# Performance work log

Hardware: AMD Instinct MI355X
Metric: run time of the kernel (lower is better)

Reference implementation:

```python
import jax, jax.numpy as jnp
import numpy as np

# Dimensions
T, B, N, E = 16, 16, 1024, 16384   # seq len, graphs per step, nodes/graph, edges/graph
F_IN, MID, H = 128, 16, 256        # node features, GCN mid channels, hidden_dim
RATIO = 0.8
K = int(np.ceil(RATIO * N))        # SAGPooling keeps K=820 nodes per graph


def setup_inputs() -> dict:
    key = jax.random.key(0)
    ks = jax.random.split(key, 16)
    def p(k, shape, s=0.05):
        return jax.random.normal(k, shape, dtype=jnp.float32) * s
    return {
        "x": jax.random.normal(ks[0], (T, B, N, F_IN), dtype=jnp.float32),
        "edge_index": jax.random.randint(ks[1], (T, B, 2, E), 0, N, dtype=jnp.int32),
        "conv1_W": p(ks[2], (F_IN, MID)),
        "conv1_b": p(ks[3], (MID,)),
        "sag_Wl": p(ks[4], (MID, 1)),   # GraphConv lin_rel (neighbor aggregate)
        "sag_Wr": p(ks[5], (MID, 1)),   # GraphConv lin_root (self)
        "sag_b": p(ks[6], (1,)),
        "conv2_W": p(ks[7], (MID, H)),
        "conv2_b": p(ks[8], (H,)),
        "W_ih": p(ks[9], (4 * H, H)),   # LSTM gates in PyTorch order i,f,g,o
        "W_hh": p(ks[10], (4 * H, H)),
        "b_ih": p(ks[11], (4 * H,)),
        "b_hh": p(ks[12], (4 * H,)),
        "cls_W": p(ks[13], (H, 1)),
        "cls_b": p(ks[14], (1,)),
    }


def _gcn(x, src, dst, w, W, b, n):
    # GCNConv with self-loops: out_i = sum_j d_i^-1/2 d_j^-1/2 w_ij (x_j W) + d_i^-1 (x_i W) + b
    h = x @ W                                            # [n, out]
    deg = jnp.ones((n,), x.dtype).at[dst].add(w)         # +1 for self-loop weight
    dinv = jax.lax.rsqrt(deg)
    coef = dinv[src] * dinv[dst] * w                     # [e]
    out = jnp.zeros_like(h).at[dst].add(h[src] * coef[:, None])
    return out + h * (dinv * dinv)[:, None] + b


def _graph_embed(x, ei, conv1_W, conv1_b, sag_Wl, sag_Wr, sag_b, conv2_W, conv2_b):
    src, dst = ei[0], ei[1]
    w = jnp.ones((E,), x.dtype)
    # conv1 + relu
    h1 = jax.nn.relu(_gcn(x, src, dst, w, conv1_W, conv1_b, N))
    # SAGPooling score via GraphConv(16 -> 1): sum-aggregate neighbors + root
    agg = jnp.zeros_like(h1).at[dst].add(h1[src])
    score = (agg @ sag_Wl + h1 @ sag_Wr + sag_b)[:, 0]   # [N]
    sv, perm = jax.lax.top_k(score, K)                   # top-k nodes
    xp = h1[perm] * jnp.tanh(sv)[:, None]                # gate kept nodes
    # remap edges to kept-node ids; drop edges touching removed nodes via zero weight
    newidx = jnp.full((N,), -1, jnp.int32).at[perm].set(jnp.arange(K, dtype=jnp.int32))
    ns, nd = newidx[src], newidx[dst]
    valid = (ns >= 0) & (nd >= 0)
    ew = valid.astype(x.dtype)
    ns = jnp.where(valid, ns, 0)
    nd = jnp.where(valid, nd, 0)
    # conv2 + relu, then global mean pool over the K kept nodes
    h2 = jax.nn.relu(_gcn(xp, ns, nd, ew, conv2_W, conv2_b, K))
    return h2.mean(axis=0)                               # [H]


def reference(x, edge_index, conv1_W, conv1_b, sag_Wl, sag_Wr, sag_b,
              conv2_W, conv2_b, W_ih, W_hh, b_ih, b_hh, cls_W, cls_b):
    embed = lambda xg, eg: _graph_embed(xg, eg, conv1_W, conv1_b,
                                        sag_Wl, sag_Wr, sag_b, conv2_W, conv2_b)
    emb = jax.vmap(jax.vmap(embed))(x, edge_index)       # [T, B, H]

    def step(carry, xt):
        h, c = carry
        g = xt @ W_ih.T + b_ih + h @ W_hh.T + b_hh
        i, f, gg, o = jnp.split(g, 4, axis=-1)
        c = jax.nn.sigmoid(f) * c + jax.nn.sigmoid(i) * jnp.tanh(gg)
        h = jax.nn.sigmoid(o) * jnp.tanh(c)
        return (h, c), None

    h0 = jnp.zeros((B, H), x.dtype)
    (hT, _), _ = jax.lax.scan(step, (h0, h0), emb)       # hT = lstm_out[:, -1, :]
    return hT @ cls_W + cls_b                            # [B, 1]
```

## Files before the change

### kernel.cpp

```cpp
#include <hip/hip_runtime.h>
#include <cmath>

#define TT 16
#define BB 16
#define NN 1024
#define EE 16384
#define FIN 128
#define MIDC 16
#define HH 256
#define KK 820
#define HS 20

#define OFF_HBUF   0
#define N_HBUF     (NN*HS)
#define OFF_CSR    (OFF_HBUF + N_HBUF)
#define N_CSR      (EE/2)
#define OFF_HEAD   (OFF_CSR + N_CSR)
#define OFF_CUR    (OFF_HEAD + NN + 1)
#define OFF_SCANA  (OFF_CUR + NN)
#define OFF_DINV   (OFF_SCANA + NN)
#define OFF_UB     (OFF_DINV + NN)
#define OFF_HIST   (OFF_UB + NN)
#define OFF_S      (OFF_HIST + 256)
#define OFF_WCNT   (OFF_S + 256)
#define OFF_CTRL   (OFF_WCNT + 16)
#define SM_FLOATS  (OFF_CTRL + 8)
#define SM_BYTES   (SM_FLOATS * 4)

__global__ __launch_bounds__(1024) void k_graph(
    const float* __restrict__ x, const int* __restrict__ ei,
    const float* __restrict__ W1, const float* __restrict__ b1,
    const float* __restrict__ Wl, const float* __restrict__ Wr,
    const float* __restrict__ bsag, const float* __restrict__ W2,
    const float* __restrict__ b2, float* __restrict__ emb)
{
  extern __shared__ __align__(16) float sm[];
  float*          hbuf  = sm + OFF_HBUF;
  float4*         hb4   = (float4*)hbuf;
  unsigned short* csr   = (unsigned short*)(sm + OFF_CSR);
  int*            head  = (int*)(sm + OFF_HEAD);
  int*            cur   = (int*)(sm + OFF_CUR);
  int*            scanA = (int*)(sm + OFF_SCANA);
  int*            scanB = (int*)(sm + OFF_DINV);
  float*          dinvb = sm + OFF_DINV;
  unsigned*       ubv   = (unsigned*)(sm + OFF_UB);
  int*            hist  = (int*)(sm + OFF_HIST);
  int*            S     = (int*)(sm + OFF_S);
  int*            wcnt  = (int*)(sm + OFF_WCNT);
  int*            ctrl  = (int*)(sm + OFF_CTRL);

  const int g   = blockIdx.x;
  const int tid = threadIdx.x;
  const float* xg   = x  + (size_t)g * (NN*FIN);
  const int*   srcp = ei + (size_t)g * (2*EE);
  const int*   dstp = srcp + EE;

  cur[tid] = 0;

  float hown[MIDC];
  {
    const float4* xr = (const float4*)(xg + (size_t)tid * FIN);
#pragma unroll
    for (int c = 0; c < MIDC; ++c) hown[c] = 0.0f;
    for (int k4 = 0; k4 < FIN/4; ++k4) {
      float4 v = xr[k4];
      const float* w0 = W1 + (k4*4 + 0)*MIDC;
      const float* w1 = W1 + (k4*4 + 1)*MIDC;
      const float* w2 = W1 + (k4*4 + 2)*MIDC;
      const float* w3 = W1 + (k4*4 + 3)*MIDC;
#pragma unroll
      for (int c = 0; c < MIDC; ++c)
        hown[c] += v.x*w0[c] + v.y*w1[c] + v.z*w2[c] + v.w*w3[c];
    }
    hb4[tid*5+0] = make_float4(hown[0],  hown[1],  hown[2],  hown[3]);
    hb4[tid*5+1] = make_float4(hown[4],  hown[5],  hown[6],  hown[7]);
    hb4[tid*5+2] = make_float4(hown[8],  hown[9],  hown[10], hown[11]);
    hb4[tid*5+3] = make_float4(hown[12], hown[13], hown[14], hown[15]);
  }
  __syncthreads();

  for (int e = tid; e < EE; e += 1024) atomicAdd(&cur[dstp[e]], 1);
  __syncthreads();

  {
    int v = cur[tid];
    scanA[tid] = v;
    __syncthreads();
    int* s_ = scanA; int* d_ = scanB;
    for (int off = 1; off < NN; off <<= 1) {
      int t = s_[tid];
      if (tid >= off) t += s_[tid - off];
      d_[tid] = t;
      __syncthreads();
      int* tmp = s_; s_ = d_; d_ = tmp;
    }
    int inc = s_[tid];
    int ex  = inc - v;
    __syncthreads();
    head[tid] = ex;
    cur[tid]  = ex;
    if (tid == 0) head[NN] = EE;
    dinvb[tid] = rsqrtf((float)(v + 1));
  }
  __syncthreads();

  for (int e = tid; e < EE; e += 1024) {
    int s = srcp[e], d = dstp[e];
    int pos = atomicAdd(&cur[d], 1);
    csr[pos] = (unsigned short)s;
  }
  __syncthreads();

  const int beg = head[tid], end = head[tid+1];

  float h1own[MIDC];
  {
    float accv[MIDC];
#pragma unroll
    for (int c = 0; c < MIDC; ++c) accv[c] = 0.0f;
    for (int p = beg; p < end; ++p) {
      int s = csr[p];
      float ds_ = dinvb[s];
      float4 a0 = hb4[s*5+0], a1 = hb4[s*5+1], a2 = hb4[s*5+2], a3 = hb4[s*5+3];
      accv[0]  += a0.x*ds_; accv[1]  += a0.y*ds_; accv[2]  += a0.z*ds_; accv[3]  += a0.w*ds_;
      accv[4]  += a1.x*ds_; accv[5]  += a1.y*ds_; accv[6]  += a1.z*ds_; accv[7]  += a1.w*ds_;
      accv[8]  += a2.x*ds_; accv[9]  += a2.y*ds_; accv[10] += a2.z*ds_; accv[11] += a2.w*ds_;
      accv[12] += a3.x*ds_; accv[13] += a3.y*ds_; accv[14] += a3.z*ds_; accv[15] += a3.w*ds_;
    }
    float di = dinvb[tid];
#pragma unroll
    for (int c = 0; c < MIDC; ++c)
      h1own[c] = fmaxf(di*accv[c] + hown[c]*di*di + b1[c], 0.0f);
  }
  __syncthreads();
  hb4[tid*5+0] = make_float4(h1own[0],  h1own[1],  h1own[2],  h1own[3]);
  hb4[tid*5+1] = make_float4(h1own[4],  h1own[5],  h1own[6],  h1own[7]);
  hb4[tid*5+2] = make_float4(h1own[8],  h1own[9],  h1own[10], h1own[11]);
  hb4[tid*5+3] = make_float4(h1own[12], h1own[13], h1own[14], h1own[15]);
  __syncthreads();

  float score;
  unsigned myu;
  {
    float aggv[MIDC];
#pragma unroll
    for (int c = 0; c < MIDC; ++c) aggv[c] = 0.0f;
    for (int p = beg; p < end; ++p) {
      int s = csr[p];
      float4 a0 = hb4[s*5+0], a1 = hb4[s*5+1], a2 = hb4[s*5+2], a3 = hb4[s*5+3];
      aggv[0]  += a0.x; aggv[1]  += a0.y; aggv[2]  += a0.z; aggv[3]  += a0.w;
      aggv[4]  += a1.x; aggv[5]  += a1.y; aggv[6]  += a1.z; aggv[7]  += a1.w;
      aggv[8]  += a2.x; aggv[9]  += a2.y; aggv[10] += a2.z; aggv[11] += a2.w;
      aggv[12] += a3.x; aggv[13] += a3.y; aggv[14] += a3.z; aggv[15] += a3.w;
    }
    score = bsag[0];
#pragma unroll
    for (int c = 0; c < MIDC; ++c) score += aggv[c]*Wl[c] + h1own[c]*Wr[c];
    unsigned ubits = __float_as_uint(score);
    myu = (ubits & 0x80000000u) ? ~ubits : (ubits | 0x80000000u);
  }

  int remK = KK;
  unsigned pref = 0;
  for (int byte = 3; byte >= 0; --byte) {
    if (tid < 256) hist[tid] = 0;
    __syncthreads();
    const int sh = byte * 8;
    const unsigned hi_mask = (byte == 3) ? 0u : (0xFFFFFFFFu << (sh + 8));
    if ((myu & hi_mask) == pref) atomicAdd(&hist[(myu >> sh) & 255u], 1);
    __syncthreads();
    if (tid < 64) {
      int h0 = hist[tid*4+0], h1_ = hist[tid*4+1], h2_ = hist[tid*4+2], h3_ = hist[tid*4+3];
      int s3 = h3_, s2 = h2_ + s3, s1 = h1_ + s2, s0 = h0 + s1;
      int run = s0;
#pragma unroll
      for (int off = 1; off < 64; off <<= 1) {
        int o = __shfl_down(run, off);
        if (tid + off < 64) run += o;
      }
      int above = run - s0;
      S[tid*4+0] = above + s0;
      S[tid*4+1] = above + s1;
      S[tid*4+2] = above + s2;
      S[tid*4+3] = above + s3;
    }
    __syncthreads();
    if (tid < 256) {
      int Sv = S[tid];
      int Sn = (tid < 255) ? S[tid+1] : 0;
      if (Sv >= remK && Sn < remK) { ctrl[0] = remK - Sn; ctrl[1] = tid; }
    }
    __syncthreads();
    remK  = ctrl[0];
    pref |= ((unsigned)ctrl[1]) << sh;
    __syncthreads();
  }
  const unsigned vstar = pref;
  const int need = remK;

  {
    const int wid = tid >> 6, lane = tid & 63;
    bool eq = (myu == vstar);
    unsigned long long m = __ballot(eq);
    if (lane == 0) wcnt[wid] = __popcll(m);
    __syncthreads();
    int before = (lane == 0) ? 0 : __popcll(m & ((~0ull) >> (64 - lane)));
    for (int w = 0; w < wid; ++w) before += wcnt[w];
    int kept = (myu > vstar) ? 1 : (eq ? (before < need) : 0);
    float gate = kept ? tanhf(score) : 0.0f;
#pragma unroll
    for (int c = 0; c < MIDC; ++c) h1own[c] *= gate;
    hb4[tid*5+0] = make_float4(h1own[0],  h1own[1],  h1own[2],  h1own[3]);
    hb4[tid*5+1] = make_float4(h1own[4],  h1own[5],  h1own[6],  h1own[7]);
    hb4[tid*5+2] = make_float4(h1own[8],  h1own[9],  h1own[10], h1own[11]);
    hb4[tid*5+3] = make_float4(h1own[12], h1own[13], h1own[14], h1own[15]);
    ubv[tid] = (unsigned)kept;
  }
  __syncthreads();

  float di2;
  {
    int cnt2 = 0;
    for (int p = beg; p < end; ++p) cnt2 += (int)ubv[csr[p]];
    di2 = rsqrtf((float)(1 + cnt2));
    dinvb[tid] = di2;
  }
  __syncthreads();

  {
    float acc2[MIDC];
#pragma unroll
    for (int c = 0; c < MIDC; ++c) acc2[c] = 0.0f;
    for (int p = beg; p < end; ++p) {
      int s = csr[p];
      float ds_ = dinvb[s];
      float4 a0 = hb4[s*5+0], a1 = hb4[s*5+1], a2 = hb4[s*5+2], a3 = hb4[s*5+3];
      acc2[0]  += a0.x*ds_; acc2[1]  += a0.y*ds_; acc2[2]  += a0.z*ds_; acc2[3]  += a0.w*ds_;
      acc2[4]  += a1.x*ds_; acc2[5]  += a1.y*ds_; acc2[6]  += a1.z*ds_; acc2[7]  += a1.w*ds_;
      acc2[8]  += a2.x*ds_; acc2[9]  += a2.y*ds_; acc2[10] += a2.z*ds_; acc2[11] += a2.w*ds_;
      acc2[12] += a3.x*ds_; acc2[13] += a3.y*ds_; acc2[14] += a3.z*ds_; acc2[15] += a3.w*ds_;
    }
#pragma unroll
    for (int c = 0; c < MIDC; ++c)
      h1own[c] = di2*acc2[c] + h1own[c]*di2*di2;
  }
  __syncthreads();
  hb4[tid*5+0] = make_float4(h1own[0],  h1own[1],  h1own[2],  h1own[3]);
  hb4[tid*5+1] = make_float4(h1own[4],  h1own[5],  h1own[6],  h1own[7]);
  hb4[tid*5+2] = make_float4(h1own[8],  h1own[9],  h1own[10], h1own[11]);
  hb4[tid*5+3] = make_float4(h1own[12], h1own[13], h1own[14], h1own[15]);
  __syncthreads();

  {
    const int ig = tid >> 6, h4 = tid & 63;
    float4 w2c[MIDC];
#pragma unroll
    for (int c = 0; c < MIDC; ++c) w2c[c] = *(const float4*)(W2 + c*HH + (h4 << 2));
    float4 bv = *(const float4*)(b2 + (h4 << 2));
    float4 pacc = make_float4(0.f, 0.f, 0.f, 0.f);
    for (int k = 0; k < 64; ++k) {
      int i = (ig << 6) + k;
      if (ubv[i] == 0u) continue;
      float4 v0 = hb4[i*5+0], v1 = hb4[i*5+1], v2 = hb4[i*5+2], v3 = hb4[i*5+3];
      float vv[MIDC] = {v0.x,v0.y,v0.z,v0.w, v1.x,v1.y,v1.z,v1.w,
                        v2.x,v2.y,v2.z,v2.w, v3.x,v3.y,v3.z,v3.w};
      float t0 = bv.x, t1 = bv.y, t2 = bv.z, t3 = bv.w;
#pragma unroll
      for (int c = 0; c < MIDC; ++c) {
        t0 += vv[c]*w2c[c].x; t1 += vv[c]*w2c[c].y;
        t2 += vv[c]*w2c[c].z; t3 += vv[c]*w2c[c].w;
      }
      pacc.x += fmaxf(t0, 0.f); pacc.y += fmaxf(t1, 0.f);
      pacc.z += fmaxf(t2, 0.f); pacc.w += fmaxf(t3, 0.f);
    }
    float4* part4 = (float4*)(sm + OFF_CSR);
    part4[(ig << 6) + h4] = pacc;
  }
  __syncthreads();
  if (tid < HH) {
    const float* part = sm + OFF_CSR;
    float s = 0.f;
#pragma unroll
    for (int ig = 0; ig < 16; ++ig) s += part[ig*HH + tid];
    emb[(size_t)g*HH + tid] = s * (1.0f/(float)KK);
  }
}

__global__ __launch_bounds__(1024) void k_gatepre(
    const float* __restrict__ emb, const float* __restrict__ W_ih,
    const float* __restrict__ b_ih, const float* __restrict__ b_hh,
    float* __restrict__ A)
{
  __shared__ __align__(16) float es[HH];
  const int g = blockIdx.x, tid = threadIdx.x;
  const int wid = tid >> 6, lane = tid & 63;
  const int sub = lane & 15, rq = lane >> 4;
  if (tid < HH) es[tid] = emb[(size_t)g*HH + tid];
  __syncthreads();
  const float4* e4 = (const float4*)es;
  for (int it = 0; it < 16; ++it) {
    const int j = it*64 + wid*4 + rq;
    const float4* wr = (const float4*)(W_ih + (size_t)j*HH);
    float p = 0.f;
#pragma unroll
    for (int kk = 0; kk < 4; ++kk) {
      float4 w = wr[sub + 16*kk];
      float4 e = e4[sub + 16*kk];
      p += w.x*e.x + w.y*e.y + w.z*e.z + w.w*e.w;
    }
    p += __shfl_xor(p, 1); p += __shfl_xor(p, 2);
    p += __shfl_xor(p, 4); p += __shfl_xor(p, 8);
    if (sub == 0) A[(size_t)g*1024 + j] = p + b_ih[j] + b_hh[j];
  }
}

__global__ __launch_bounds__(256) void k_step(
    const float* __restrict__ A_t, const float* __restrict__ W_hh,
    const float* __restrict__ h_in, float* __restrict__ h_out,
    float* __restrict__ cbuf)
{
  __shared__ __align__(16) float hsh[HH];
  __shared__ float gl[16][4];
  const int b = blockIdx.x >> 4, ug = blockIdx.x & 15;
  const int tid = threadIdx.x;
  const int ul = tid >> 4, sub = tid & 15;
  if (tid < HH) hsh[tid] = h_in[b*HH + tid];
  __syncthreads();
  const float4* h4 = (const float4*)hsh;
  float4 hv0 = h4[sub], hv1 = h4[sub+16], hv2 = h4[sub+32], hv3 = h4[sub+48];
  const int u = ug*16 + ul;
  float gv[4];
#pragma unroll
  for (int gg_ = 0; gg_ < 4; ++gg_) {
    const float4* wr = (const float4*)(W_hh + (size_t)(gg_*HH + u)*HH);
    float4 w0 = wr[sub], w1 = wr[sub+16], w2 = wr[sub+32], w3 = wr[sub+48];
    float p = w0.x*hv0.x + w0.y*hv0.y + w0.z*hv0.z + w0.w*hv0.w
            + w1.x*hv1.x + w1.y*hv1.y + w1.z*hv1.z + w1.w*hv1.w
            + w2.x*hv2.x + w2.y*hv2.y + w2.z*hv2.z + w2.w*hv2.w
            + w3.x*hv3.x + w3.y*hv3.y + w3.z*hv3.z + w3.w*hv3.w;
    p += __shfl_xor(p, 1); p += __shfl_xor(p, 2);
    p += __shfl_xor(p, 4); p += __shfl_xor(p, 8);
    gv[gg_] = p;
  }
  if (sub == 0) { gl[ul][0]=gv[0]; gl[ul][1]=gv[1]; gl[ul][2]=gv[2]; gl[ul][3]=gv[3]; }
  __syncthreads();
  if (tid < 16) {
    const int uu = ug*16 + tid;
    const float* At = A_t + b*1024;
    float gi = gl[tid][0] + At[uu      ];
    float gf = gl[tid][1] + At[uu + 256];
    float gn = gl[tid][2] + At[uu + 512];
    float go = gl[tid][3] + At[uu + 768];
    float iv = 1.0f/(1.0f + expf(-gi));
    float fv = 1.0f/(1.0f + expf(-gf));
    float gvv = tanhf(gn);
    float ov = 1.0f/(1.0f + expf(-go));
    float c = fv * cbuf[b*HH + uu] + iv * gvv;
    cbuf[b*HH + uu] = c;
    h_out[b*HH + uu] = ov * tanhf(c);
  }
}

__global__ __launch_bounds__(256) void k_cls(
    const float* __restrict__ h, const float* __restrict__ cls_W,
    const float* __restrict__ cls_b, float* __restrict__ out)
{
  __shared__ float red[4];
  const int b = blockIdx.x, tid = threadIdx.x;
  float p = h[b*HH + tid] * cls_W[tid];
#pragma unroll
  for (int off = 32; off >= 1; off >>= 1) p += __shfl_down(p, off);
  if ((tid & 63) == 0) red[tid >> 6] = p;
  __syncthreads();
  if (tid == 0) out[b] = red[0] + red[1] + red[2] + red[3] + cls_b[0];
}

extern "C" void kernel_launch(void* const* d_in, const int* in_sizes, int n_in,
                              void* d_out, int out_size, void* d_ws, size_t ws_size,
                              hipStream_t stream)
{
  const float* x    = (const float*)d_in[0];
  const int*   ei   = (const int*)  d_in[1];
  const float* W1   = (const float*)d_in[2];
  const float* b1   = (const float*)d_in[3];
  const float* Wl   = (const float*)d_in[4];
  const float* Wr   = (const float*)d_in[5];
  const float* bs   = (const float*)d_in[6];
  const float* W2   = (const float*)d_in[7];
  const float* b2   = (const float*)d_in[8];
  const float* Wih  = (const float*)d_in[9];
  const float* Whh  = (const float*)d_in[10];
  const float* bih  = (const float*)d_in[11];
  const float* bhh  = (const float*)d_in[12];
  const float* clsW = (const float*)d_in[13];
  const float* clsb = (const float*)d_in[14];
  float* out = (float*)d_out;

  float* emb = (float*)d_ws;
  float* A   = emb + (size_t)TT*BB*HH;
  float* hA  = emb;
  float* hB  = emb + BB*HH;
  float* cb  = emb + 2*BB*HH;

  (void)hipFuncSetAttribute(reinterpret_cast<const void*>(k_graph),
      hipFuncAttributeMaxDynamicSharedMemorySize, SM_BYTES);

  hipLaunchKernelGGL(k_graph, dim3(TT*BB), dim3(1024), SM_BYTES, stream,
                     x, ei, W1, b1, Wl, Wr, bs, W2, b2, emb);
  hipLaunchKernelGGL(k_gatepre, dim3(TT*BB), dim3(1024), 0, stream,
                     emb, Wih, bih, bhh, A);
  (void)hipMemsetAsync(hA, 0, BB*HH*sizeof(float), stream);
  (void)hipMemsetAsync(cb, 0, BB*HH*sizeof(float), stream);
  for (int t = 0; t < TT; ++t) {
    const float* hin  = (t & 1) ? hB : hA;
    float*       hout = (t & 1) ? hA : hB;
    hipLaunchKernelGGL(k_step, dim3(256), dim3(256), 0, stream,
                       A + (size_t)t*BB*1024, Whh, hin, hout, cb);
  }
  hipLaunchKernelGGL(k_cls, dim3(BB), dim3(256), 0, stream, hA, clsW, clsb, out);
}
```

Baseline: 423.2 us.

## Split conv1 into bf16 kernel and fuse LSTM into persistent grid-barrier kernel

The x@W1 projection moves out of the graph kernel into a separate fully parallel kernel that writes bf16-packed results. The graph kernel then reads 32 bytes per node instead of recomputing the projection from 512 bytes. The gate precompute, the 16 LSTM step launches and the classifier are merged into one persistent kernel that keeps W_ih/W_hh rows in registers and syncs with a software grid barrier, removing about 18 launches. Risks: bf16 rounding of h1 may change which nodes top-k selects, and the grid barrier assumes all 256 blocks are co-resident.

```diff
diff --git a/kernel.cpp b/kernel.cpp
--- a/kernel.cpp
+++ b/kernel.cpp
@@ -27,16 +27,56 @@
 #define SM_FLOATS  (OFF_CTRL + 8)
 #define SM_BYTES   (SM_FLOATS * 4)
 
+__device__ __forceinline__ unsigned bf16pair(float a, float b) {
+  unsigned ua = __float_as_uint(a), ub_ = __float_as_uint(b);
+  ua  = (ua  + 0x7FFFu + ((ua  >> 16) & 1u)) >> 16;
+  ub_ = (ub_ + 0x7FFFu + ((ub_ >> 16) & 1u)) >> 16;
+  return ua | (ub_ << 16);
+}
+__device__ __forceinline__ float bf16lo(unsigned p) { return __uint_as_float(p << 16); }
+__device__ __forceinline__ float bf16hi(unsigned p) { return __uint_as_float(p & 0xFFFF0000u); }
+__device__ __forceinline__ float dot4(float4 a, float4 b) {
+  return a.x*b.x + a.y*b.y + a.z*b.z + a.w*b.w;
+}
+
+__global__ __launch_bounds__(256) void k_conv1(
+    const float* __restrict__ x, const float* __restrict__ W1,
+    unsigned* __restrict__ h0)
+{
+  const int gid = blockIdx.x * 256 + threadIdx.x;
+  const float4* xr = (const float4*)(x + (size_t)gid * FIN);
+  float acc[MIDC];
+#pragma unroll
+  for (int c = 0; c < MIDC; ++c) acc[c] = 0.0f;
+  for (int k4 = 0; k4 < FIN/4; ++k4) {
+    float4 v = xr[k4];
+    const float* w0 = W1 + (k4*4 + 0)*MIDC;
+    const float* w1 = W1 + (k4*4 + 1)*MIDC;
+    const float* w2 = W1 + (k4*4 + 2)*MIDC;
+    const float* w3 = W1 + (k4*4 + 3)*MIDC;
+#pragma unroll
+    for (int c = 0; c < MIDC; ++c)
+      acc[c] += v.x*w0[c] + v.y*w1[c] + v.z*w2[c] + v.w*w3[c];
+  }
+  uint4 q0, q1;
+  q0.x = bf16pair(acc[0],  acc[1]);  q0.y = bf16pair(acc[2],  acc[3]);
+  q0.z = bf16pair(acc[4],  acc[5]);  q0.w = bf16pair(acc[6],  acc[7]);
+  q1.x = bf16pair(acc[8],  acc[9]);  q1.y = bf16pair(acc[10], acc[11]);
+  q1.z = bf16pair(acc[12], acc[13]); q1.w = bf16pair(acc[14], acc[15]);
+  uint4* o = (uint4*)h0;
+  o[(size_t)gid*2 + 0] = q0;
+  o[(size_t)gid*2 + 1] = q1;
+}
+
 __global__ __launch_bounds__(1024) void k_graph(
-    const float* __restrict__ x, const int* __restrict__ ei,
-    const float* __restrict__ W1, const float* __restrict__ b1,
+    const unsigned* __restrict__ h0, const int* __restrict__ ei,
+    const float* __restrict__ b1,
     const float* __restrict__ Wl, const float* __restrict__ Wr,
     const float* __restrict__ bsag, const float* __restrict__ W2,
     const float* __restrict__ b2, float* __restrict__ emb)
 {
   extern __shared__ __align__(16) float sm[];
-  float*          hbuf  = sm + OFF_HBUF;
-  float4*         hb4   = (float4*)hbuf;
+  float4*         hb4   = (float4*)(sm + OFF_HBUF);
   unsigned short* csr   = (unsigned short*)(sm + OFF_CSR);
   int*            head  = (int*)(sm + OFF_HEAD);
   int*            cur   = (int*)(sm + OFF_CUR);
@@ -51,7 +91,6 @@
 
   const int g   = blockIdx.x;
   const int tid = threadIdx.x;
-  const float* xg   = x  + (size_t)g * (NN*FIN);
   const int*   srcp = ei + (size_t)g * (2*EE);
   const int*   dstp = srcp + EE;
 
@@ -59,19 +98,16 @@
 
   float hown[MIDC];
   {
-    const float4* xr = (const float4*)(xg + (size_t)tid * FIN);
-#pragma unroll
-    for (int c = 0; c < MIDC; ++c) hown[c] = 0.0f;
-    for (int k4 = 0; k4 < FIN/4; ++k4) {
-      float4 v = xr[k4];
-      const float* w0 = W1 + (k4*4 + 0)*MIDC;
-      const float* w1 = W1 + (k4*4 + 1)*MIDC;
-      const float* w2 = W1 + (k4*4 + 2)*MIDC;
-      const float* w3 = W1 + (k4*4 + 3)*MIDC;
-#pragma unroll
-      for (int c = 0; c < MIDC; ++c)
-        hown[c] += v.x*w0[c] + v.y*w1[c] + v.z*w2[c] + v.w*w3[c];
-    }
+    const uint4* hp = (const uint4*)h0 + (size_t)g * NN * 2;
+    uint4 p0 = hp[tid*2], p1 = hp[tid*2 + 1];
+    hown[0] = bf16lo(p0.x); hown[1] = bf16hi(p0.x);
+    hown[2] = bf16lo(p0.y); hown[3] = bf16hi(p0.y);
+    hown[4] = bf16lo(p0.z); hown[5] = bf16hi(p0.z);
+    hown[6] = bf16lo(p0.w); hown[7] = bf16hi(p0.w);
+    hown[8]  = bf16lo(p1.x); hown[9]  = bf16hi(p1.x);
+    hown[10] = bf16lo(p1.y); hown[11] = bf16hi(p1.y);
+    hown[12] = bf16lo(p1.z); hown[13] = bf16hi(p1.z);
+    hown[14] = bf16lo(p1.w); hown[15] = bf16hi(p1.w);
     hb4[tid*5+0] = make_float4(hown[0],  hown[1],  hown[2],  hown[3]);
     hb4[tid*5+1] = make_float4(hown[4],  hown[5],  hown[6],  hown[7]);
     hb4[tid*5+2] = make_float4(hown[8],  hown[9],  hown[10], hown[11]);
@@ -170,8 +206,8 @@
     if ((myu & hi_mask) == pref) atomicAdd(&hist[(myu >> sh) & 255u], 1);
     __syncthreads();
     if (tid < 64) {
-      int h0 = hist[tid*4+0], h1_ = hist[tid*4+1], h2_ = hist[tid*4+2], h3_ = hist[tid*4+3];
-      int s3 = h3_, s2 = h2_ + s3, s1 = h1_ + s2, s0 = h0 + s1;
+      int h0_ = hist[tid*4+0], h1_ = hist[tid*4+1], h2_ = hist[tid*4+2], h3_ = hist[tid*4+3];
+      int s3 = h3_, s2 = h2_ + s3, s1 = h1_ + s2, s0 = h0_ + s1;
       int run = s0;
 #pragma unroll
       for (int off = 1; off < 64; off <<= 1) {
@@ -286,93 +322,110 @@
   }
 }
 
-__global__ __launch_bounds__(1024) void k_gatepre(
+__device__ __forceinline__ void grid_barrier(unsigned* bar, unsigned nblk) {
+  __syncthreads();
+  if (threadIdx.x == 0) {
+    __threadfence();
+    unsigned g0 = __hip_atomic_load(bar + 1, __ATOMIC_RELAXED, __HIP_MEMORY_SCOPE_AGENT);
+    unsigned arr = __hip_atomic_fetch_add(bar, 1u, __ATOMIC_ACQ_REL, __HIP_MEMORY_SCOPE_AGENT);
+    if (arr == nblk - 1u) {
+      __hip_atomic_store(bar, 0u, __ATOMIC_RELAXED, __HIP_MEMORY_SCOPE_AGENT);
+      __hip_atomic_fetch_add(bar + 1, 1u, __ATOMIC_RELEASE, __HIP_MEMORY_SCOPE_AGENT);
+    } else {
+      while (__hip_atomic_load(bar + 1, __ATOMIC_ACQUIRE, __HIP_MEMORY_SCOPE_AGENT) == g0)
+        __builtin_amdgcn_s_sleep(8);
+    }
+    __threadfence();
+  }
+  __syncthreads();
+}
+
+__global__ __launch_bounds__(256) void k_lstm_all(
     const float* __restrict__ emb, const float* __restrict__ W_ih,
     const float* __restrict__ b_ih, const float* __restrict__ b_hh,
-    float* __restrict__ A)
+    const float* __restrict__ W_hh, const float* __restrict__ clsW,
+    const float* __restrict__ clsb, float* __restrict__ hA,
+    float* __restrict__ hB, unsigned* __restrict__ bar,
+    float* __restrict__ out)
 {
-  __shared__ __align__(16) float es[HH];
-  const int g = blockIdx.x, tid = threadIdx.x;
-  const int wid = tid >> 6, lane = tid & 63;
-  const int sub = lane & 15, rq = lane >> 4;
-  if (tid < HH) es[tid] = emb[(size_t)g*HH + tid];
-  __syncthreads();
-  const float4* e4 = (const float4*)es;
-  for (int it = 0; it < 16; ++it) {
-    const int j = it*64 + wid*4 + rq;
-    const float4* wr = (const float4*)(W_ih + (size_t)j*HH);
-    float p = 0.f;
-#pragma unroll
-    for (int kk = 0; kk < 4; ++kk) {
-      float4 w = wr[sub + 16*kk];
-      float4 e = e4[sub + 16*kk];
-      p += w.x*e.x + w.y*e.y + w.z*e.z + w.w*e.w;
-    }
-    p += __shfl_xor(p, 1); p += __shfl_xor(p, 2);
-    p += __shfl_xor(p, 4); p += __shfl_xor(p, 8);
-    if (sub == 0) A[(size_t)g*1024 + j] = p + b_ih[j] + b_hh[j];
-  }
-}
-
-__global__ __launch_bounds__(256) void k_step(
-    const float* __restrict__ A_t, const float* __restrict__ W_hh,
-    const float* __restrict__ h_in, float* __restrict__ h_out,
-    float* __restrict__ cbuf)
-{
-  __shared__ __align__(16) float hsh[HH];
-  __shared__ float gl[16][4];
-  const int b = blockIdx.x >> 4, ug = blockIdx.x & 15;
-  const int tid = threadIdx.x;
-  const int ul = tid >> 4, sub = tid & 15;
-  if (tid < HH) hsh[tid] = h_in[b*HH + tid];
-  __syncthreads();
-  const float4* h4 = (const float4*)hsh;
-  float4 hv0 = h4[sub], hv1 = h4[sub+16], hv2 = h4[sub+32], hv3 = h4[sub+48];
+  __shared__ float Ablk[TT][4][16];
+  __shared__ float redsc[4];
+  const int bid = blockIdx.x, b = bid >> 4, ug = bid & 15;
+  const int tid = threadIdx.x, ul = tid >> 4, sub = tid & 15;
   const int u = ug*16 + ul;
-  float gv[4];
-#pragma unroll
-  for (int gg_ = 0; gg_ < 4; ++gg_) {
-    const float4* wr = (const float4*)(W_hh + (size_t)(gg_*HH + u)*HH);
-    float4 w0 = wr[sub], w1 = wr[sub+16], w2 = wr[sub+32], w3 = wr[sub+48];
-    float p = w0.x*hv0.x + w0.y*hv0.y + w0.z*hv0.z + w0.w*hv0.w
-            + w1.x*hv1.x + w1.y*hv1.y + w1.z*hv1.z + w1.w*hv1.w
-            + w2.x*hv2.x + w2.y*hv2.y + w2.z*hv2.z + w2.w*hv2.w
-            + w3.x*hv3.x + w3.y*hv3.y + w3.z*hv3.z + w3.w*hv3.w;
-    p += __shfl_xor(p, 1); p += __shfl_xor(p, 2);
-    p += __shfl_xor(p, 4); p += __shfl_xor(p, 8);
-    gv[gg_] = p;
-  }
-  if (sub == 0) { gl[ul][0]=gv[0]; gl[ul][1]=gv[1]; gl[ul][2]=gv[2]; gl[ul][3]=gv[3]; }
-  __syncthreads();
-  if (tid < 16) {
-    const int uu = ug*16 + tid;
-    const float* At = A_t + b*1024;
-    float gi = gl[tid][0] + At[uu      ];
-    float gf = gl[tid][1] + At[uu + 256];
-    float gn = gl[tid][2] + At[uu + 512];
-    float go = gl[tid][3] + At[uu + 768];
-    float iv = 1.0f/(1.0f + expf(-gi));
-    float fv = 1.0f/(1.0f + expf(-gf));
-    float gvv = tanhf(gn);
-    float ov = 1.0f/(1.0f + expf(-go));
-    float c = fv * cbuf[b*HH + uu] + iv * gvv;
-    cbuf[b*HH + uu] = c;
-    h_out[b*HH + uu] = ov * tanhf(c);
-  }
-}
-
-__global__ __launch_bounds__(256) void k_cls(
-    const float* __restrict__ h, const float* __restrict__ cls_W,
-    const float* __restrict__ cls_b, float* __restrict__ out)
-{
-  __shared__ float red[4];
-  const int b = blockIdx.x, tid = threadIdx.x;
-  float p = h[b*HH + tid] * cls_W[tid];
-#pragma unroll
-  for (int off = 32; off >= 1; off >>= 1) p += __shfl_down(p, off);
-  if ((tid & 63) == 0) red[tid >> 6] = p;
-  __syncthreads();
-  if (tid == 0) out[b] = red[0] + red[1] + red[2] + red[3] + cls_b[0];
+
+  {
+    float4 wih[4][4];
+#pragma unroll
+    for (int g = 0; g < 4; ++g) {
+      const float4* wr = (const float4*)(W_ih + (size_t)(g*HH + u)*HH) + sub*4;
+#pragma unroll
+      for (int k = 0; k < 4; ++k) wih[g][k] = wr[k];
+    }
+    for (int t = 0; t < TT; ++t) {
+      const float4* e4 = (const float4*)(emb + (size_t)(t*BB + b)*HH) + sub*4;
+      float4 e0 = e4[0], e1 = e4[1], e2 = e4[2], e3 = e4[3];
+#pragma unroll
+      for (int g = 0; g < 4; ++g) {
+        float p = dot4(wih[g][0],e0) + dot4(wih[g][1],e1)
+                + dot4(wih[g][2],e2) + dot4(wih[g][3],e3);
+        p += __shfl_xor(p, 1); p += __shfl_xor(p, 2);
+        p += __shfl_xor(p, 4); p += __shfl_xor(p, 8);
+        if (sub == 0) Ablk[t][g][ul] = p + b_ih[g*HH + u] + b_hh[g*HH + u];
+      }
+    }
+  }
+
+  float4 whh[4][4];
+#pragma unroll
+  for (int g = 0; g < 4; ++g) {
+    const float4* wr = (const float4*)(W_hh + (size_t)(g*HH + u)*HH) + sub*4;
+#pragma unroll
+    for (int k = 0; k < 4; ++k) whh[g][k] = wr[k];
+  }
+  __syncthreads();
+
+  float cst = 0.0f;
+  for (int t = 0; t < TT; ++t) {
+    float pg0 = 0.f, pg1 = 0.f, pg2 = 0.f, pg3 = 0.f;
+    if (t > 0) {
+      const float* hprev = (t & 1) ? hA : hB;
+      const float4* h4 = (const float4*)(hprev + b*HH) + sub*4;
+      float4 h0v = h4[0], h1v = h4[1], h2v = h4[2], h3v = h4[3];
+      pg0 = dot4(whh[0][0],h0v)+dot4(whh[0][1],h1v)+dot4(whh[0][2],h2v)+dot4(whh[0][3],h3v);
+      pg1 = dot4(whh[1][0],h0v)+dot4(whh[1][1],h1v)+dot4(whh[1][2],h2v)+dot4(whh[1][3],h3v);
+      pg2 = dot4(whh[2][0],h0v)+dot4(whh[2][1],h1v)+dot4(whh[2][2],h2v)+dot4(whh[2][3],h3v);
+      pg3 = dot4(whh[3][0],h0v)+dot4(whh[3][1],h1v)+dot4(whh[3][2],h2v)+dot4(whh[3][3],h3v);
+#pragma unroll
+      for (int off = 1; off < 16; off <<= 1) {
+        pg0 += __shfl_xor(pg0, off); pg1 += __shfl_xor(pg1, off);
+        pg2 += __shfl_xor(pg2, off); pg3 += __shfl_xor(pg3, off);
+      }
+    }
+    if (sub == 0) {
+      float gi = pg0 + Ablk[t][0][ul];
+      float gf = pg1 + Ablk[t][1][ul];
+      float gn = pg2 + Ablk[t][2][ul];
+      float go = pg3 + Ablk[t][3][ul];
+      float iv = 1.0f/(1.0f + expf(-gi));
+      float fv = 1.0f/(1.0f + expf(-gf));
+      float gv = tanhf(gn);
+      float ov = 1.0f/(1.0f + expf(-go));
+      cst = fv*cst + iv*gv;
+      float* hw = (t & 1) ? hB : hA;
+      hw[b*HH + u] = ov * tanhf(cst);
+    }
+    grid_barrier(bar, 256u);
+  }
+
+  if (ug == 0) {
+    float p = hB[b*HH + tid] * clsW[tid];
+#pragma unroll
+    for (int off = 32; off >= 1; off >>= 1) p += __shfl_down(p, off);
+    if ((tid & 63) == 0) redsc[tid >> 6] = p;
+    __syncthreads();
+    if (tid == 0) out[b] = redsc[0] + redsc[1] + redsc[2] + redsc[3] + clsb[0];
+  }
 }
 
 extern "C" void kernel_launch(void* const* d_in, const int* in_sizes, int n_in,
@@ -396,26 +449,20 @@
   const float* clsb = (const float*)d_in[14];
   float* out = (float*)d_out;
 
-  float* emb = (float*)d_ws;
-  float* A   = emb + (size_t)TT*BB*HH;
-  float* hA  = emb;
-  float* hB  = emb + BB*HH;
-  float* cb  = emb + 2*BB*HH;
+  unsigned* h0  = (unsigned*)d_ws;
+  float*    emb = (float*)(h0 + (size_t)TT*BB*NN*8);
+  float*    hA  = emb + (size_t)TT*BB*HH;
+  float*    hB  = hA + BB*HH;
+  unsigned* bar = (unsigned*)(hB + BB*HH);
 
   (void)hipFuncSetAttribute(reinterpret_cast<const void*>(k_graph),
       hipFuncAttributeMaxDynamicSharedMemorySize, SM_BYTES);
 
+  (void)hipMemsetAsync(bar, 0, 2*sizeof(unsigned), stream);
+  hipLaunchKernelGGL(k_conv1, dim3(TT*BB*NN/256), dim3(256), 0, stream,
+                     x, W1, h0);
   hipLaunchKernelGGL(k_graph, dim3(TT*BB), dim3(1024), SM_BYTES, stream,
-                     x, ei, W1, b1, Wl, Wr, bs, W2, b2, emb);
-  hipLaunchKernelGGL(k_gatepre, dim3(TT*BB), dim3(1024), 0, stream,
-                     emb, Wih, bih, bhh, A);
-  (void)hipMemsetAsync(hA, 0, BB*HH*sizeof(float), stream);
-  (void)hipMemsetAsync(cb, 0, BB*HH*sizeof(float), stream);
-  for (int t = 0; t < TT; ++t) {
-    const float* hin  = (t & 1) ? hB : hA;
-    float*       hout = (t & 1) ? hA : hB;
-    hipLaunchKernelGGL(k_step, dim3(256), dim3(256), 0, stream,
-                       A + (size_t)t*BB*1024, Whh, hin, hout, cb);
-  }
-  hipLaunchKernelGGL(k_cls, dim3(BB), dim3(256), 0, stream, hA, clsW, clsb, out);
-}
+                     h0, ei, b1, Wl, Wr, bs, W2, b2, emb);
+  hipLaunchKernelGGL(k_lstm_all, dim3(256), dim3(256), 0, stream,
+                     emb, Wih, bih, bhh, Whh, clsW, clsb, hA, hB, bar, out);
+}
```

After: 782.0 us. +84.8%, slower.
